# Kernel tuning notes

Measured on AMD Instinct MI355X. Metric: run time of the kernel, lower is better.

The kernel has to match this reference:

```python
import jax, jax.numpy as jnp
import numpy as np

N, E, F0, HEADS, B, OUT = 100000, 1600000, 128, 4, 64, 32
CHANNELS = [16, 8, 4, 2]
NEG_SLOPE = 0.2


def setup_inputs() -> dict:
    key = jax.random.key(0)
    ks = jax.random.split(key, 40)
    inp = {}
    inp['x'] = jax.random.normal(ks[0], (N, F0), dtype=jnp.float32)
    inp['edge_index'] = jax.random.randint(ks[1], (2, E), 0, N, dtype=jnp.int64)
    inp['batch'] = jnp.sort(jax.random.randint(ks[2], (N,), 0, B, dtype=jnp.int64))
    # GATConv params per layer: W [in, heads*out], att_src/att_dst [heads, out], bias [heads*out]
    in_dim = F0
    ki = 3
    for li, oc in enumerate(CHANNELS, start=1):
        scale = 1.0 / np.sqrt(in_dim)
        inp[f'W{li}'] = jax.random.normal(ks[ki], (in_dim, HEADS * oc), dtype=jnp.float32) * scale
        inp[f'a_src{li}'] = jax.random.normal(ks[ki + 1], (HEADS, oc), dtype=jnp.float32) * 0.1
        inp[f'a_dst{li}'] = jax.random.normal(ks[ki + 2], (HEADS, oc), dtype=jnp.float32) * 0.1
        inp[f'b{li}'] = jnp.zeros((HEADS * oc,), dtype=jnp.float32)
        ki += 3
        in_dim = HEADS * oc
    inp['W_fc'] = jax.random.normal(ks[ki], (2 * HEADS, OUT), dtype=jnp.float32) * (1.0 / np.sqrt(2 * HEADS))
    inp['b_fc'] = jnp.zeros((OUT,), dtype=jnp.float32)
    return inp


def gat_layer(x, src, dst, W, a_src, a_dst, b, oc):
    n = x.shape[0]
    h = (x @ W).reshape(n, HEADS, oc)                    # [N, H, C]
    al_s = jnp.einsum('nhc,hc->nh', h, a_src)            # [N, H]
    al_d = jnp.einsum('nhc,hc->nh', h, a_dst)
    e = jax.nn.leaky_relu(al_s[src] + al_d[dst], NEG_SLOPE)  # [E, H]
    # segment softmax over incoming edges per destination node
    m = jax.ops.segment_max(e, dst, num_segments=n)
    m = jnp.where(jnp.isfinite(m), m, 0.0)
    ex = jnp.exp(e - m[dst])
    s = jax.ops.segment_sum(ex, dst, num_segments=n)
    alpha = ex / (s[dst] + 1e-16)                        # [E, H]
    out = jax.ops.segment_sum(h[src] * alpha[:, :, None], dst, num_segments=n)
    return out.reshape(n, HEADS * oc) + b


def reference(x, edge_index, batch, W1, a_src1, a_dst1, b1, W2, a_src2, a_dst2, b2,
              W3, a_src3, a_dst3, b3, W4, a_src4, a_dst4, b4, W_fc, b_fc):
    n = x.shape[0]
    loops = jnp.arange(n, dtype=edge_index.dtype)
    src = jnp.concatenate([edge_index[0], loops])   # PyG GATConv adds self-loops
    dst = jnp.concatenate([edge_index[1], loops])
    params = [(W1, a_src1, a_dst1, b1), (W2, a_src2, a_dst2, b2),
              (W3, a_src3, a_dst3, b3), (W4, a_src4, a_dst4, b4)]
    h = x
    for (W, a_s, a_d, b), oc in zip(params, CHANNELS):
        h = jax.nn.relu(gat_layer(h, src, dst, W, a_s, a_d, b, oc))
        # dropout(0.3) is identity at inference
    # global mean pool over graphs in the batch
    sums = jax.ops.segment_sum(h, batch, num_segments=B)
    cnt = jax.ops.segment_sum(jnp.ones((n,), h.dtype), batch, num_segments=B)
    pooled = sums / jnp.maximum(cnt, 1.0)[:, None]
    return pooled @ W_fc + b_fc
```

## Files before the change

### kernel.cpp

```cpp
#include <hip/hip_runtime.h>
#include <hip/hip_bf16.h>

#define NNODES 100000
#define NEDGES 1600000
#define NHEADS 4
#define NGRAPH 64
#define NOUTF  32
#define BSH    9
#define NBUK   ((NNODES + 511) >> 9)
#define BPAD   16
#define BCAP   9216
#define CGRID  512
#define G1GRID ((NNODES + 63) / 64)

__device__ __forceinline__ unsigned short f2bf(float f) {
    union { float f; unsigned u; } v;
    v.f = f;
    unsigned r = v.u + 0x7FFF + ((v.u >> 16) & 1);
    return (unsigned short)(r >> 16);
}
__device__ __forceinline__ float bflo(unsigned u) {
    union { unsigned u; float f; } v;
    v.u = u << 16;
    return v.f;
// ... 40 lines not shown
            int d = wide ? ei[2 * (ne + i)] : ei[ne + i];
            atomicAdd(&hist[d >> BSH], 1);
        }
        __syncthreads();
        for (int i = tid; i < NBUK; i += 256)
            base[i] = hist[i] ? atomicAdd(&bkcur[i * BPAD], hist[i]) : 0;
        __syncthreads();
        for (int i = tid; i < NBUK; i += 256) hist[i] = 0;
        __syncthreads();
        for (int i = e0 + tid; i < e1; i += 256) {
            int s = wide ? ei[2 * i] : ei[i];
            int d = wide ? ei[2 * (ne + i)] : ei[ne + i];
            int bk = d >> BSH;
            int pos = base[bk] + atomicAdd(&hist[bk], 1);
            if (pos < BCAP) packed[bk * BCAP + pos] = s | ((d & 511) << 17);
        }
        int gid = blockIdx.x * 256 + tid;
        for (int i = gid; i < n; i += CGRID * 256) bat[i] = wide ? bt[2 * i] : bt[i];
    } else {
        constexpr int DIN = 128, DOUT = 64, KTILE = 64;
        constexpr int OG = DOUT / 4;
        constexpr int NPB = 64;
        constexpr int S = DIN + 4;
        constexpr int C = DOUT / NHEADS;
        float* Wl = smem;
        float* xs = smem + KTILE * DOUT;
        const int base = (blockIdx.x - CGRID) * NPB;
        constexpr int KC = DIN / 4;
        for (int i = tid; i < NPB * KC; i += 256) {
            int nn = i / KC, kc = i - nn * KC;
            int nd = base + nn;
            float4 v = (nd < n) ? ((const float4*)x)[(size_t)nd * KC + kc]
                                : make_float4(0.f, 0.f, 0.f, 0.f);
            *(float4*)&xs[nn * S + kc * 4] = v;
        }
        const int og = tid % OG;
        const int ng = tid / OG;
        const int n0 = ng * 4;
        float4 acc[4] = {};
        for (int kt = 0; kt < DIN; kt += KTILE) {
            __syncthreads();
            for (int i = tid; i < KTILE * OG; i += 256)
                ((float4*)Wl)[i] = ((const float4*)W1)[kt * OG + i];
            __syncthreads();
            #pragma unroll 2
            for (int k = 0; k < KTILE; k += 4) {
                float4 wv[4], xv[4];
                #pragma unroll
                for (int j = 0; j < 4; j++)
                    wv[j] = *(const float4*)&Wl[(k + j) * DOUT + og * 4];
                #pragma unroll
                for (int r = 0; r < 4; r++)
                    xv[r] = *(const float4*)&xs[(n0 + r) * S + kt + k];
                #pragma unroll
                for (int r = 0; r < 4; r++) {
                    fma4(acc[r], xv[r].x, wv[0]);
                    fma4(acc[r], xv[r].y, wv[1]);
                    fma4(acc[r], xv[r].z, wv[2]);
                    fma4(acc[r], xv[r].w, wv[3]);
                }
            }
        }
        float4 asv = ((const float4*)as1)[og];
        float4 adv = ((const float4*)ad1)[og];
        #pragma unroll
        for (int r = 0; r < 4; r++) {
            int node = base + n0 + r;
            bool ok = node < n;
            if (ok) {
                ushort4 o;
                o.x = f2bf(acc[r].x);
                o.y = f2bf(acc[r].y);
                o.z = f2bf(acc[r].z);
                o.w = f2bf(acc[r].w);
                ((ushort4*)h1)[(size_t)node * OG + og] = o;
            }
            float ps = acc[r].x * asv.x + acc[r].y * asv.y + acc[r].z * asv.z + acc[r].w * asv.w;
            float pd = acc[r].x * adv.x + acc[r].y * adv.y + acc[r].z * adv.z + acc[r].w * adv.w;
            #pragma unroll
            for (int off = 1; off < C / 4; off <<= 1) {
                ps += __shfl_xor(ps, off);
                pd += __shfl_xor(pd, off);
            }
            if (ok && (og % (C / 4)) == 0) {
                int hh = og / (C / 4);
                al_s[node * NHEADS + hh] = ps;
                al_d[node * NHEADS + hh] = pd;
            }
        }
    }
}

__global__ __launch_bounds__(1024) void gat_fine_kernel(
        const int* __restrict__ packed, const int* __restrict__ bkcur,
        int* __restrict__ row_ptr, int* __restrict__ col, int n) {
    __shared__ int bscan[256];
    __shared__ int dg[512];
    __shared__ int excl[512];
    __shared__ int partial[256];
    __shared__ int cur[512];
    int b = blockIdx.x;
    int tid = threadIdx.x;
    if (tid < 256) bscan[tid] = (tid < NBUK) ? bkcur[tid * BPAD] : 0;
    if (tid < 512) dg[tid] = 0;
    __syncthreads();
    for (int off = 1; off < 256; off <<= 1) {
        int u = (tid < 256 && tid >= off) ? bscan[tid - off] : 0;
        __syncthreads();
        if (tid < 256) bscan[tid] += u;
        __syncthreads();
    }
    int cntb = bkcur[b * BPAD];
    int csr0 = bscan[b] - cntb;
    int pbeg = b * BCAP;
    int pend = pbeg + cntb;
    for (int t = pbeg + tid; t < pend; t += 1024)
        atomicAdd(&dg[packed[t] >> 17], 1);
    __syncthreads();
    int a0 = 0, a1 = 0, s = 0;
    if (tid < 256) {
        a0 = dg[2 * tid];
        a1 = dg[2 * tid + 1];
        s = a0 + a1;
        partial[tid] = s;
    }
    __syncthreads();
    for (int off = 1; off < 256; off <<= 1) {
        int u = (tid < 256 && tid >= off) ? partial[tid - off] : 0;
        __syncthreads();
        if (tid < 256) partial[tid] += u;
        __syncthreads();
    }
    if (tid < 256) {
        int ebase = partial[tid] - s;
        excl[2 * tid] = ebase;
        excl[2 * tid + 1] = ebase + a0;
        cur[2 * tid] = ebase;
        cur[2 * tid + 1] = ebase + a0;
    }
    __syncthreads();
    int node0 = b << BSH;
    if (tid < 512) {
        int nd = node0 + tid;
        if (nd < n) row_ptr[nd] = csr0 + excl[tid];
    }
    if (b == NBUK - 1 && tid == 0) row_ptr[n] = bscan[NBUK - 1];
    for (int t = pbeg + tid; t < pend; t += 1024) {
        int v = packed[t];
        int pos = atomicAdd(&cur[v >> 17], 1);
        col[csr0 + pos] = v & 0x1FFFF;
    }
}

template<int DIN, int DOUT, int KTILE, bool BF16OUT, int STRIDE>
__global__ __launch_bounds__(256) void gat_gemm_attn_kernel(
        const float* __restrict__ in, const float* __restrict__ W,
        const float* __restrict__ a_src, const float* __restrict__ a_dst,
        char* __restrict__ hrow, float* __restrict__ al_d, int n) {
    constexpr int OG = DOUT / 4;
    constexpr int NPB = 1024 / OG;
    constexpr int S = DIN + 4;
    constexpr int C = DOUT / NHEADS;
    __shared__ float Wl[KTILE * DOUT];
    __shared__ float xs[NPB * S];
    const int tid = threadIdx.x;
    const int base = blockIdx.x * NPB;
    constexpr int KC = DIN / 4;
    for (int i = tid; i < NPB * KC; i += 256) {
        int nn = i / KC, kc = i - nn * KC;
        int nd = base + nn;
        float4 v = (nd < n) ? ((const float4*)in)[(size_t)nd * KC + kc]
                            : make_float4(0.f, 0.f, 0.f, 0.f);
        *(float4*)&xs[nn * S + kc * 4] = v;
    }
    const int og = tid % OG;
    const int ng = tid / OG;
    const int n0 = ng * 4;
    float4 acc[4] = {};
    for (int kt = 0; kt < DIN; kt += KTILE) {
        __syncthreads();
        for (int i = tid; i < KTILE * OG; i += 256)
            ((float4*)Wl)[i] = ((const float4*)W)[kt * OG + i];
        __syncthreads();
        #pragma unroll 2
        for (int k = 0; k < KTILE; k += 4) {
            float4 wv[4], xv[4];
            #pragma unroll
            for (int j = 0; j < 4; j++)
                wv[j] = *(const float4*)&Wl[(k + j) * DOUT + og * 4];
            #pragma unroll
            for (int r = 0; r < 4; r++)
                xv[r] = *(const float4*)&xs[(n0 + r) * S + kt + k];
            #pragma unroll
            for (int r = 0; r < 4; r++) {
                fma4(acc[r], xv[r].x, wv[0]);
                fma4(acc[r], xv[r].y, wv[1]);
                fma4(acc[r], xv[r].z, wv[2]);
                fma4(acc[r], xv[r].w, wv[3]);
            }
        }
    }
    float4 asv = ((const float4*)a_src)[og];
    float4 adv = ((const float4*)a_dst)[og];
    #pragma unroll
    for (int r = 0; r < 4; r++) {
        int node = base + n0 + r;
        bool ok = node < n;
        char* rp = hrow + (size_t)node * STRIDE;
        if (ok) {
            if constexpr (BF16OUT) {
                ushort4 o;
                o.x = f2bf(acc[r].x);
                o.y = f2bf(acc[r].y);
                o.z = f2bf(acc[r].z);
                o.w = f2bf(acc[r].w);
                *(ushort4*)(rp + 16 + og * 8) = o;
            } else {
                *(float4*)(rp + 16 + og * 16) = acc[r];
            }
        }
        if constexpr (C >= 4) {
            float ps = acc[r].x * asv.x + acc[r].y * asv.y + acc[r].z * asv.z + acc[r].w * asv.w;
            float pd = acc[r].x * adv.x + acc[r].y * adv.y + acc[r].z * adv.z + acc[r].w * adv.w;
            #pragma unroll
            for (int off = 1; off < C / 4; off <<= 1) {
                ps += __shfl_xor(ps, off);
                pd += __shfl_xor(pd, off);
            }
            if (ok && (og % (C / 4)) == 0) {
                int hh = og / (C / 4);
                *(float*)(rp + 4 * hh) = ps;
                al_d[node * NHEADS + hh] = pd;
            }
        } else {
            if (ok) {
                *(float*)(rp + 8 * og)     = acc[r].x * asv.x + acc[r].y * asv.y;
                *(float*)(rp + 8 * og + 4) = acc[r].z * asv.z + acc[r].w * asv.w;
                al_d[node * NHEADS + 2 * og]     = acc[r].x * adv.x + acc[r].y * adv.y;
                al_d[node * NHEADS + 2 * og + 1] = acc[r].z * adv.z + acc[r].w * adv.w;
            }
        }
    }
}

template<int G>
__global__ __launch_bounds__(256) void gat_agg_group_kernel(
        const unsigned short* __restrict__ h, const float* __restrict__ al_s,
        const float* __restrict__ al_d, const int* __restrict__ row_ptr,
        const int* __restrict__ col, const float* __restrict__ bias,
        float* __restrict__ out, int n) {
    constexpr int L = G / 8;
    constexpr int PW = 64 / L;
    constexpr int C = G / NHEADS;
    int lane = threadIdx.x & 63;
    int sub = lane & (L - 1);
    int gidx = lane / L;
    int node = blockIdx.x * (4 * PW) + (threadIdx.x >> 6) * PW + gidx;
    if (node >= n) return;
    int beg = row_ptr[node];
    int cnt = row_ptr[node + 1] - beg;
    const uint4* h4 = (const uint4*)h;
    float acc[8] = {};
    int j0 = sub * 8;
    const int hh = (sub * 8) / C;
    float ald = al_d[node * NHEADS + hh];
    float ws = 0.f;
    int total = cnt + 1;
    int t = 0;
    for (; t + 2 <= total; t += 2) {
        int s0 = col[beg + t];
        int s1 = (t + 1 < cnt) ? col[beg + t + 1] : node;
        float e0 = al_s[s0 * NHEADS + hh] + ald;
        float e1 = al_s[s1 * NHEADS + hh] + ald;
        uint4 hv0 = h4[(size_t)s0 * L + sub];
        uint4 hv1 = h4[(size_t)s1 * L + sub];
        e0 = (e0 > 0.f) ? e0 : 0.2f * e0;
        e1 = (e1 > 0.f) ? e1 : 0.2f * e1;
        float w0 = __expf(e0);
        float w1 = __expf(e1);
        ws += w0;
        acc[0] += w0 * bflo(hv0.x);
        acc[1] += w0 * bfhi(hv0.x);
        acc[2] += w0 * bflo(hv0.y);
        acc[3] += w0 * bfhi(hv0.y);
        acc[4] += w0 * bflo(hv0.z);
        acc[5] += w0 * bfhi(hv0.z);
        acc[6] += w0 * bflo(hv0.w);
        acc[7] += w0 * bfhi(hv0.w);
        ws += w1;
        acc[0] += w1 * bflo(hv1.x);
        acc[1] += w1 * bfhi(hv1.x);
        acc[2] += w1 * bflo(hv1.y);
        acc[3] += w1 * bfhi(hv1.y);
        acc[4] += w1 * bflo(hv1.z);
        acc[5] += w1 * bfhi(hv1.z);
        acc[6] += w1 * bflo(hv1.w);
        acc[7] += w1 * bfhi(hv1.w);
    }
    if (t < total) {
        int s0 = (t < cnt) ? col[beg + t] : node;
        float e0 = al_s[s0 * NHEADS + hh] + ald;
        uint4 hv0 = h4[(size_t)s0 * L + sub];
        e0 = (e0 > 0.f) ? e0 : 0.2f * e0;
        float w0 = __expf(e0);
        ws += w0;
        acc[0] += w0 * bflo(hv0.x);
        acc[1] += w0 * bfhi(hv0.x);
        acc[2] += w0 * bflo(hv0.y);
        acc[3] += w0 * bfhi(hv0.y);
        acc[4] += w0 * bflo(hv0.z);
        acc[5] += w0 * bfhi(hv0.z);
        acc[6] += w0 * bflo(hv0.w);
        acc[7] += w0 * bfhi(hv0.w);
    }
    float inv = 1.f / (ws + 1e-16f);
    #pragma unroll
    for (int k = 0; k < 8; k++) acc[k] = acc[k] * inv + bias[j0 + k];
    float4 o0, o1;
    o0.x = (acc[0] > 0.f) ? acc[0] : 0.f;
    o0.y = (acc[1] > 0.f) ? acc[1] : 0.f;
    o0.z = (acc[2] > 0.f) ? acc[2] : 0.f;
    o0.w = (acc[3] > 0.f) ? acc[3] : 0.f;
    o1.x = (acc[4] > 0.f) ? acc[4] : 0.f;
    o1.y = (acc[5] > 0.f) ? acc[5] : 0.f;
    o1.z = (acc[6] > 0.f) ? acc[6] : 0.f;
    o1.w = (acc[7] > 0.f) ? acc[7] : 0.f;
    *(float4*)&out[(size_t)node * G + j0] = o0;
    *(float4*)&out[(size_t)node * G + j0 + 4] = o1;
}

template<int G, int STRIDE>
__global__ __launch_bounds__(256) void gat_agg_row_kernel(
        const char* __restrict__ hrow, const float* __restrict__ al_d,
        const int* __restrict__ row_ptr, const int* __restrict__ col,
        const float* __restrict__ bias, float* __restrict__ out, int n) {
    constexpr int L = G / 8;
    constexpr int PW = 64 / L;
    constexpr int C = G / NHEADS;
    int lane = threadIdx.x & 63;
    int sub = lane & (L - 1);
    int gidx = lane / L;
    int node = blockIdx.x * (4 * PW) + (threadIdx.x >> 6) * PW + gidx;
    if (node >= n) return;
    int beg = row_ptr[node];
    int cnt = row_ptr[node + 1] - beg;
    float acc[8] = {};
    int j0 = sub * 8;
    if constexpr (C >= 8) {
        const int hh = sub;
        float ald = al_d[node * NHEADS + hh];
        float ws = 0.f;
        int total = cnt + 1;
        int t = 0;
        for (; t + 2 <= total; t += 2) {
            int s0 = col[beg + t];
            int s1 = (t + 1 < cnt) ? col[beg + t + 1] : node;
            const char* r0 = hrow + (size_t)s0 * STRIDE;
            const char* r1 = hrow + (size_t)s1 * STRIDE;
            float e0 = *(const float*)(r0 + 4 * hh) + ald;
            float e1 = *(const float*)(r1 + 4 * hh) + ald;
            uint4 hv0 = *(const uint4*)(r0 + 16 + 16 * sub);
            uint4 hv1 = *(const uint4*)(r1 + 16 + 16 * sub);
            e0 = (e0 > 0.f) ? e0 : 0.2f * e0;
            e1 = (e1 > 0.f) ? e1 : 0.2f * e1;
            float w0 = __expf(e0);
            float w1 = __expf(e1);
            ws += w0;
            acc[0] += w0 * bflo(hv0.x);
            acc[1] += w0 * bfhi(hv0.x);
            acc[2] += w0 * bflo(hv0.y);
            acc[3] += w0 * bfhi(hv0.y);
            acc[4] += w0 * bflo(hv0.z);
            acc[5] += w0 * bfhi(hv0.z);
            acc[6] += w0 * bflo(hv0.w);
            acc[7] += w0 * bfhi(hv0.w);
            ws += w1;
            acc[0] += w1 * bflo(hv1.x);
            acc[1] += w1 * bfhi(hv1.x);
            acc[2] += w1 * bflo(hv1.y);
            acc[3] += w1 * bfhi(hv1.y);
            acc[4] += w1 * bflo(hv1.z);
            acc[5] += w1 * bfhi(hv1.z);
            acc[6] += w1 * bflo(hv1.w);
            acc[7] += w1 * bfhi(hv1.w);
        }
        if (t < total) {
            int s0 = (t < cnt) ? col[beg + t] : node;
            const char* r0 = hrow + (size_t)s0 * STRIDE;
            float e0 = *(const float*)(r0 + 4 * hh) + ald;
            uint4 hv0 = *(const uint4*)(r0 + 16 + 16 * sub);
            e0 = (e0 > 0.f) ? e0 : 0.2f * e0;
            float w0 = __expf(e0);
            ws += w0;
            acc[0] += w0 * bflo(hv0.x);
            acc[1] += w0 * bfhi(hv0.x);
            acc[2] += w0 * bflo(hv0.y);
            acc[3] += w0 * bfhi(hv0.y);
            acc[4] += w0 * bflo(hv0.z);
            acc[5] += w0 * bfhi(hv0.z);
            acc[6] += w0 * bflo(hv0.w);
            acc[7] += w0 * bfhi(hv0.w);
        }
        float inv = 1.f / (ws + 1e-16f);
        #pragma unroll
        for (int k = 0; k < 8; k++) acc[k] = acc[k] * inv + bias[j0 + k];
    } else {
        const int hh0 = 2 * sub, hh1 = 2 * sub + 1;
        float ald0 = al_d[node * NHEADS + hh0];
        float ald1 = al_d[node * NHEADS + hh1];
        float ws0 = 0.f, ws1 = 0.f;
        int total = cnt + 1;
        int t = 0;
        for (; t + 2 <= total; t += 2) {
            int s0 = col[beg + t];
            int s1 = (t + 1 < cnt) ? col[beg + t + 1] : node;
            const char* r0 = hrow + (size_t)s0 * STRIDE;
            const char* r1 = hrow + (size_t)s1 * STRIDE;
            float2 a0 = *(const float2*)(r0 + 8 * sub);
            float2 a1 = *(const float2*)(r1 + 8 * sub);
            uint4 hv0 = *(const uint4*)(r0 + 16 + 16 * sub);
            uint4 hv1 = *(const uint4*)(r1 + 16 + 16 * sub);
            float e00 = a0.x + ald0;
            float e01 = a0.y + ald1;
            float e10 = a1.x + ald0;
            float e11 = a1.y + ald1;
            e00 = (e00 > 0.f) ? e00 : 0.2f * e00;
            e01 = (e01 > 0.f) ? e01 : 0.2f * e01;
            e10 = (e10 > 0.f) ? e10 : 0.2f * e10;
            e11 = (e11 > 0.f) ? e11 : 0.2f * e11;
            float w00 = __expf(e00);
            float w01 = __expf(e01);
            float w10 = __expf(e10);
            float w11 = __expf(e11);
            ws0 += w00;
            ws1 += w01;
            acc[0] += w00 * bflo(hv0.x);
            acc[1] += w00 * bfhi(hv0.x);
            acc[2] += w00 * bflo(hv0.y);
            acc[3] += w00 * bfhi(hv0.y);
            acc[4] += w01 * bflo(hv0.z);
            acc[5] += w01 * bfhi(hv0.z);
            acc[6] += w01 * bflo(hv0.w);
            acc[7] += w01 * bfhi(hv0.w);
            ws0 += w10;
            ws1 += w11;
            acc[0] += w10 * bflo(hv1.x);
            acc[1] += w10 * bfhi(hv1.x);
            acc[2] += w10 * bflo(hv1.y);
            acc[3] += w10 * bfhi(hv1.y);
            acc[4] += w11 * bflo(hv1.z);
            acc[5] += w11 * bfhi(hv1.z);
            acc[6] += w11 * bflo(hv1.w);
            acc[7] += w11 * bfhi(hv1.w);
        }
        if (t < total) {
            int s0 = (t < cnt) ? col[beg + t] : node;
            const char* r0 = hrow + (size_t)s0 * STRIDE;
            float2 a0 = *(const float2*)(r0 + 8 * sub);
            uint4 hv0 = *(const uint4*)(r0 + 16 + 16 * sub);
            float e00 = a0.x + ald0;
            float e01 = a0.y + ald1;
            e00 = (e00 > 0.f) ? e00 : 0.2f * e00;
            e01 = (e01 > 0.f) ? e01 : 0.2f * e01;
            float w00 = __expf(e00);
            float w01 = __expf(e01);
            ws0 += w00;
            ws1 += w01;
            acc[0] += w00 * bflo(hv0.x);
            acc[1] += w00 * bfhi(hv0.x);
            acc[2] += w00 * bflo(hv0.y);
            acc[3] += w00 * bfhi(hv0.y);
            acc[4] += w01 * bflo(hv0.z);
            acc[5] += w01 * bfhi(hv0.z);
            acc[6] += w01 * bflo(hv0.w);
            acc[7] += w01 * bfhi(hv0.w);
        }
        float inv0 = 1.f / (ws0 + 1e-16f);
        float inv1 = 1.f / (ws1 + 1e-16f);
        #pragma unroll
        for (int k = 0; k < 4; k++) acc[k] = acc[k] * inv0 + bias[j0 + k];
        #pragma unroll
        for (int k = 4; k < 8; k++) acc[k] = acc[k] * inv1 + bias[j0 + k];
    }
    float4 o0, o1;
    o0.x = (acc[0] > 0.f) ? acc[0] : 0.f;
    o0.y = (acc[1] > 0.f) ? acc[1] : 0.f;
    o0.z = (acc[2] > 0.f) ? acc[2] : 0.f;
    o0.w = (acc[3] > 0.f) ? acc[3] : 0.f;
    o1.x = (acc[4] > 0.f) ? acc[4] : 0.f;
    o1.y = (acc[5] > 0.f) ? acc[5] : 0.f;
    o1.z = (acc[6] > 0.f) ? acc[6] : 0.f;
    o1.w = (acc[7] > 0.f) ? acc[7] : 0.f;
    *(float4*)&out[(size_t)node * G + j0] = o0;
    *(float4*)&out[(size_t)node * G + j0 + 4] = o1;
}

__global__ __launch_bounds__(256) void gat_agg_f32row_kernel(
        const char* __restrict__ hrow, const float* __restrict__ al_d,
        const int* __restrict__ row_ptr, const int* __restrict__ col,
        const float* __restrict__ bias, float* __restrict__ out, int n) {
    constexpr int L = 2;
    constexpr int PW = 32;
    int lane = threadIdx.x & 63;
    int sub = lane & 1;
    int gidx = lane >> 1;
    int node = blockIdx.x * (4 * PW) + (threadIdx.x >> 6) * PW + gidx;
    if (node >= n) return;
    int beg = row_ptr[node];
    int cnt = row_ptr[node + 1] - beg;
    const int hh0 = 2 * sub, hh1 = 2 * sub + 1;
    float ald0 = al_d[node * NHEADS + hh0];
    float ald1 = al_d[node * NHEADS + hh1];
    float4 acc = make_float4(0.f, 0.f, 0.f, 0.f);
    float ws0 = 0.f, ws1 = 0.f;
    int total = cnt + 1;
    int t = 0;
    for (; t + 2 <= total; t += 2) {
        int s0 = col[beg + t];
        int s1 = (t + 1 < cnt) ? col[beg + t + 1] : node;
        const char* r0 = hrow + (size_t)s0 * 64;
        const char* r1 = hrow + (size_t)s1 * 64;
        float2 a0 = *(const float2*)(r0 + 8 * sub);
        float2 a1 = *(const float2*)(r1 + 8 * sub);
        float4 hv0 = *(const float4*)(r0 + 16 + 16 * sub);
        float4 hv1 = *(const float4*)(r1 + 16 + 16 * sub);
        float e00 = a0.x + ald0;
        float e01 = a0.y + ald1;
        float e10 = a1.x + ald0;
        float e11 = a1.y + ald1;
        e00 = (e00 > 0.f) ? e00 : 0.2f * e00;
        e01 = (e01 > 0.f) ? e01 : 0.2f * e01;
        e10 = (e10 > 0.f) ? e10 : 0.2f * e10;
        e11 = (e11 > 0.f) ? e11 : 0.2f * e11;
        float w00 = __expf(e00);
        float w01 = __expf(e01);
        float w10 = __expf(e10);
        float w11 = __expf(e11);
        ws0 += w00;
        ws1 += w01;
        acc.x += w00 * hv0.x;
        acc.y += w00 * hv0.y;
        acc.z += w01 * hv0.z;
        acc.w += w01 * hv0.w;
        ws0 += w10;
        ws1 += w11;
        acc.x += w10 * hv1.x;
        acc.y += w10 * hv1.y;
        acc.z += w11 * hv1.z;
        acc.w += w11 * hv1.w;
    }
    if (t < total) {
        int s0 = (t < cnt) ? col[beg + t] : node;
        const char* r0 = hrow + (size_t)s0 * 64;
        float2 a0 = *(const float2*)(r0 + 8 * sub);
        float4 hv0 = *(const float4*)(r0 + 16 + 16 * sub);
        float e00 = a0.x + ald0;
        float e01 = a0.y + ald1;
        e00 = (e00 > 0.f) ? e00 : 0.2f * e00;
        e01 = (e01 > 0.f) ? e01 : 0.2f * e01;
        float w00 = __expf(e00);
        float w01 = __expf(e01);
        ws0 += w00;
        ws1 += w01;
        acc.x += w00 * hv0.x;
        acc.y += w00 * hv0.y;
        acc.z += w01 * hv0.z;
        acc.w += w01 * hv0.w;
    }
    float4 bv = ((const float4*)bias)[sub];
    float4 v;
    v.x = acc.x / (ws0 + 1e-16f) + bv.x;
    v.y = acc.y / (ws0 + 1e-16f) + bv.y;
    v.z = acc.z / (ws1 + 1e-16f) + bv.z;
    v.w = acc.w / (ws1 + 1e-16f) + bv.w;
    v.x = (v.x > 0.f) ? v.x : 0.f;
    v.y = (v.y > 0.f) ? v.y : 0.f;
    v.z = (v.z > 0.f) ? v.z : 0.f;
    v.w = (v.w > 0.f) ? v.w : 0.f;
    ((float4*)out)[(size_t)node * L + sub] = v;
}

__global__ __launch_bounds__(256) void gat_poolfc_kernel(
        const float* __restrict__ x, const int* __restrict__ bat,
        const float* __restrict__ Wfc, const float* __restrict__ bfc,
        float* __restrict__ out, int n) {
    __shared__ float sh[256][9];
    int b = blockIdx.x;
    int tid = threadIdx.x;
    int lo = 0, hi = n;
    while (lo < hi) { int mid = (lo + hi) >> 1; if (bat[mid] < b) lo = mid + 1; else hi = mid; }
    int i0 = lo;
    hi = n;
    while (lo < hi) { int mid = (lo + hi) >> 1; if (bat[mid] < b + 1) lo = mid + 1; else hi = mid; }
    int i1 = lo;
    float a[8] = {};
    for (int i = i0 + tid; i < i1; i += 256) {
        float4 v0 = ((const float4*)x)[(size_t)i * 2];
        float4 v1 = ((const float4*)x)[(size_t)i * 2 + 1];
        a[0] += v0.x; a[1] += v0.y; a[2] += v0.z; a[3] += v0.w;
        a[4] += v1.x; a[5] += v1.y; a[6] += v1.z; a[7] += v1.w;
    }
    #pragma unroll
    for (int k = 0; k < 8; k++) sh[tid][k] = a[k];
    __syncthreads();
    for (int off = 128; off >= 1; off >>= 1) {
        if (tid < off)
            #pragma unroll
            for (int k = 0; k < 8; k++) sh[tid][k] += sh[tid + off][k];
        __syncthreads();
    }
    if (tid < NOUTF) {
        float c = (float)(i1 - i0);
        if (c < 1.f) c = 1.f;
        float acc = bfc[tid];
        #pragma unroll
        for (int d = 0; d < 8; d++) acc += (sh[0][d] / c) * Wfc[d * NOUTF + tid];
        out[b * NOUTF + tid] = acc;
    }
}

extern "C" void kernel_launch(void* const* d_in, const int* in_sizes, int n_in,
                              void* d_out, int out_size, void* d_ws, size_t ws_size,
                              hipStream_t stream) {
    const float* x = (const float*)d_in[0];
    const int* ei = (const int*)d_in[1];
    const int* batch = (const int*)d_in[2];
    const float* W1 = (const float*)d_in[3];
    const float* as1 = (const float*)d_in[4];
    const float* ad1 = (const float*)d_in[5];
    const float* b1 = (const float*)d_in[6];
    const float* W2 = (const float*)d_in[7];
    const float* as2 = (const float*)d_in[8];
    const float* ad2 = (const float*)d_in[9];
    const float* b2 = (const float*)d_in[10];
    const float* W3 = (const float*)d_in[11];
    const float* as3 = (const float*)d_in[12];
    const float* ad3 = (const float*)d_in[13];
    const float* b3 = (const float*)d_in[14];
    const float* W4 = (const float*)d_in[15];
    const float* as4 = (const float*)d_in[16];
    const float* ad4 = (const float*)d_in[17];
    const float* b4 = (const float*)d_in[18];
    const float* Wfc = (const float*)d_in[19];
    const float* bfc = (const float*)d_in[20];

    const int n = NNODES, ne = NEDGES;

    char* p = (char*)d_ws;
    auto carve = [&](size_t bytes) {
        char* r = p;
        p += (bytes + 255) & ~(size_t)255;
        return r;
    };
    int* row_ptr = (int*)carve((size_t)(n + 1) * 4);
    int* col = (int*)carve((size_t)ne * 4);
    int* bkcur = (int*)carve(256 * BPAD * 4);
    int* packed = (int*)carve((size_t)NBUK * BCAP * 4);
    float* buf_h = (float*)carve((size_t)n * 64 * 4);
    float* buf_x = (float*)carve((size_t)n * 64 * 4);
    float* al_s = (float*)carve((size_t)n * NHEADS * 4);
    float* al_d = (float*)carve((size_t)n * NHEADS * 4);
    int* bat = (int*)carve((size_t)n * 4);
    unsigned short* h_bf16 = (unsigned short*)buf_h;
    char* hrow = (char*)buf_h;

    hipMemsetAsync(bkcur, 0, 256 * BPAD * 4, stream);

    gat_coarse_gemm1_kernel<<<CGRID + G1GRID, 256, 0, stream>>>(
        ei, batch, bkcur, packed, bat, x, W1, as1, ad1, h_bf16, al_s, al_d, ne, n);

    gat_fine_kernel<<<NBUK, 1024, 0, stream>>>(packed, bkcur, row_ptr, col, n);

    gat_agg_group_kernel<64><<<(n + 31) / 32, 256, 0, stream>>>(
        h_bf16, al_s, al_d, row_ptr, col, b1, buf_x, n);

    gat_gemm_attn_kernel<64, 32, 64, true, 96><<<(n + 127) / 128, 256, 0, stream>>>(
        buf_x, W2, as2, ad2, hrow, al_d, n);
    gat_agg_row_kernel<32, 96><<<(n + 63) / 64, 256, 0, stream>>>(
        hrow, al_d, row_ptr, col, b2, buf_x, n);

    gat_gemm_attn_kernel<32, 16, 32, true, 64><<<(n + 255) / 256, 256, 0, stream>>>(
        buf_x, W3, as3, ad3, hrow, al_d, n);
    gat_agg_row_kernel<16, 64><<<(n + 127) / 128, 256, 0, stream>>>(
        hrow, al_d, row_ptr, col, b3, buf_x, n);

    gat_gemm_attn_kernel<16, 8, 16, false, 64><<<(n + 511) / 512, 256, 0, stream>>>(
        buf_x, W4, as4, ad4, hrow, al_d, n);
    gat_agg_f32row_kernel<<<(n + 127) / 128, 256, 0, stream>>>(
        hrow, al_d, row_ptr, col, b4, buf_x, n);

    gat_poolfc_kernel<<<NGRAPH, 256, 0, stream>>>(buf_x, bat, Wfc, bfc, (float*)d_out, n);
}
```

Measured before the change: 381.1 us.

## Fuse each layer's aggregation with the next layer's projection GEMM

Each layer's neighbour-aggregation kernel is merged with the following layer's dense projection and attention-logit computation. The aggregated, ReLU'd node row is written to shared memory and multiplied by the next weight matrix, which is also staged in shared memory. This removes the write and re-read of the intermediate activations in global memory and drops three kernel launches. In exchange the small GEMMs lose their cross-node register tiling. Output buffers now alternate between the two workspace buffers so a kernel never reads and writes the same one.

```diff
diff --git a/kernel.cpp b/kernel.cpp
--- a/kernel.cpp
+++ b/kernel.cpp
@@ -216,128 +216,44 @@
     }
 }
 
-template<int DIN, int DOUT, int KTILE, bool BF16OUT, int STRIDE>
-__global__ __launch_bounds__(256) void gat_gemm_attn_kernel(
-        const float* __restrict__ in, const float* __restrict__ W,
-        const float* __restrict__ a_src, const float* __restrict__ a_dst,
-        char* __restrict__ hrow, float* __restrict__ al_d, int n) {
-    constexpr int OG = DOUT / 4;
-    constexpr int NPB = 1024 / OG;
-    constexpr int S = DIN + 4;
-    constexpr int C = DOUT / NHEADS;
-    __shared__ float Wl[KTILE * DOUT];
-    __shared__ float xs[NPB * S];
+__global__ __launch_bounds__(256) void gat_agg1_gemm2_kernel(
+        const unsigned short* __restrict__ h, const float* __restrict__ al_s,
+        const float* __restrict__ al_d_l1, const int* __restrict__ row_ptr,
+        const int* __restrict__ col, const float* __restrict__ b1,
+        const float* __restrict__ W2, const float* __restrict__ as2,
+        const float* __restrict__ ad2, char* __restrict__ hrow_out,
+        float* __restrict__ al_d, int n) {
+    __shared__ float Wl[64 * 32];
+    __shared__ float xs[32 * 68];
     const int tid = threadIdx.x;
-    const int base = blockIdx.x * NPB;
-    constexpr int KC = DIN / 4;
-    for (int i = tid; i < NPB * KC; i += 256) {
-        int nn = i / KC, kc = i - nn * KC;
-        int nd = base + nn;
-        float4 v = (nd < n) ? ((const float4*)in)[(size_t)nd * KC + kc]
-                            : make_float4(0.f, 0.f, 0.f, 0.f);
-        *(float4*)&xs[nn * S + kc * 4] = v;
-    }
-    const int og = tid % OG;
-    const int ng = tid / OG;
-    const int n0 = ng * 4;
-    float4 acc[4] = {};
-    for (int kt = 0; kt < DIN; kt += KTILE) {
-        __syncthreads();
-        for (int i = tid; i < KTILE * OG; i += 256)
-            ((float4*)Wl)[i] = ((const float4*)W)[kt * OG + i];
-        __syncthreads();
-        #pragma unroll 2
-        for (int k = 0; k < KTILE; k += 4) {
-            float4 wv[4], xv[4];
-            #pragma unroll
-            for (int j = 0; j < 4; j++)
-                wv[j] = *(const float4*)&Wl[(k + j) * DOUT + og * 4];
-            #pragma unroll
-            for (int r = 0; r < 4; r++)
-                xv[r] = *(const float4*)&xs[(n0 + r) * S + kt + k];
-            #pragma unroll
-            for (int r = 0; r < 4; r++) {
-                fma4(acc[r], xv[r].x, wv[0]);
-                fma4(acc[r], xv[r].y, wv[1]);
-                fma4(acc[r], xv[r].z, wv[2]);
-                fma4(acc[r], xv[r].w, wv[3]);
-            }
-        }
-    }
-    float4 asv = ((const float4*)a_src)[og];
-    float4 adv = ((const float4*)a_dst)[og];
-    #pragma unroll
-    for (int r = 0; r < 4; r++) {
-        int node = base + n0 + r;
-        bool ok = node < n;
-        char* rp = hrow + (size_t)node * STRIDE;
-        if (ok) {
-            if constexpr (BF16OUT) {
-                ushort4 o;
-                o.x = f2bf(acc[r].x);
-                o.y = f2bf(acc[r].y);
-                o.z = f2bf(acc[r].z);
-                o.w = f2bf(acc[r].w);
-                *(ushort4*)(rp + 16 + og * 8) = o;
-            } else {
-                *(float4*)(rp + 16 + og * 16) = acc[r];
-            }
-        }
-        if constexpr (C >= 4) {
-            float ps = acc[r].x * asv.x + acc[r].y * asv.y + acc[r].z * asv.z + acc[r].w * asv.w;
-            float pd = acc[r].x * adv.x + acc[r].y * adv.y + acc[r].z * adv.z + acc[r].w * adv.w;
-            #pragma unroll
-            for (int off = 1; off < C / 4; off <<= 1) {
-                ps += __shfl_xor(ps, off);
-                pd += __shfl_xor(pd, off);
-            }
-            if (ok && (og % (C / 4)) == 0) {
-                int hh = og / (C / 4);
-                *(float*)(rp + 4 * hh) = ps;
-                al_d[node * NHEADS + hh] = pd;
-            }
-        } else {
-            if (ok) {
-                *(float*)(rp + 8 * og)     = acc[r].x * asv.x + acc[r].y * asv.y;
-                *(float*)(rp + 8 * og + 4) = acc[r].z * asv.z + acc[r].w * asv.w;
-                al_d[node * NHEADS + 2 * og]     = acc[r].x * adv.x + acc[r].y * adv.y;
-                al_d[node * NHEADS + 2 * og + 1] = acc[r].z * adv.z + acc[r].w * adv.w;
-            }
-        }
-    }
-}
-
-template<int G>
-__global__ __launch_bounds__(256) void gat_agg_group_kernel(
-        const unsigned short* __restrict__ h, const float* __restrict__ al_s,
-        const float* __restrict__ al_d, const int* __restrict__ row_ptr,
-        const int* __restrict__ col, const float* __restrict__ bias,
-        float* __restrict__ out, int n) {
-    constexpr int L = G / 8;
-    constexpr int PW = 64 / L;
-    constexpr int C = G / NHEADS;
-    int lane = threadIdx.x & 63;
-    int sub = lane & (L - 1);
-    int gidx = lane / L;
-    int node = blockIdx.x * (4 * PW) + (threadIdx.x >> 6) * PW + gidx;
-    if (node >= n) return;
-    int beg = row_ptr[node];
-    int cnt = row_ptr[node + 1] - beg;
+    for (int i = tid; i < 64 * 32 / 4; i += 256)
+        ((float4*)Wl)[i] = ((const float4*)W2)[i];
+    __syncthreads();
+    int lane = tid & 63;
+    int sub = lane & 7;
+    int gidx = lane >> 3;
+    int slot = (tid >> 6) * 8 + gidx;
+    int node = blockIdx.x * 32 + slot;
+    bool ok = node < n;
+    int node_c = ok ? node : (n - 1);
+    int beg = row_ptr[node_c];
+    int cnt = row_ptr[node_c + 1] - beg;
     const uint4* h4 = (const uint4*)h;
     float acc[8] = {};
     int j0 = sub * 8;
-    const int hh = (sub * 8) / C;
-    float ald = al_d[node * NHEADS + hh];
+    float ald = al_d_l1[node_c * NHEADS + sub];
+    ald = al_d_l1[node_c * NHEADS + (sub >> 1)];
+    const int hh = sub >> 1;
     float ws = 0.f;
     int total = cnt + 1;
     int t = 0;
     for (; t + 2 <= total; t += 2) {
         int s0 = col[beg + t];
-        int s1 = (t + 1 < cnt) ? col[beg + t + 1] : node;
+        int s1 = (t + 1 < cnt) ? col[beg + t + 1] : node_c;
         float e0 = al_s[s0 * NHEADS + hh] + ald;
         float e1 = al_s[s1 * NHEADS + hh] + ald;
-        uint4 hv0 = h4[(size_t)s0 * L + sub];
-        uint4 hv1 = h4[(size_t)s1 * L + sub];
+        uint4 hv0 = h4[(size_t)s0 * 8 + sub];
+        uint4 hv1 = h4[(size_t)s1 * 8 + sub];
         e0 = (e0 > 0.f) ? e0 : 0.2f * e0;
         e1 = (e1 > 0.f) ? e1 : 0.2f * e1;
         float w0 = __expf(e0);
@@ -362,9 +278,9 @@
         acc[7] += w1 * bfhi(hv1.w);
     }
     if (t < total) {
-        int s0 = (t < cnt) ? col[beg + t] : node;
+        int s0 = (t < cnt) ? col[beg + t] : node_c;
         float e0 = al_s[s0 * NHEADS + hh] + ald;
-        uint4 hv0 = h4[(size_t)s0 * L + sub];
+        uint4 hv0 = h4[(size_t)s0 * 8 + sub];
         e0 = (e0 > 0.f) ? e0 : 0.2f * e0;
         float w0 = __expf(e0);
         ws += w0;
@@ -379,184 +295,297 @@
     }
     float inv = 1.f / (ws + 1e-16f);
     #pragma unroll
-    for (int k = 0; k < 8; k++) acc[k] = acc[k] * inv + bias[j0 + k];
-    float4 o0, o1;
-    o0.x = (acc[0] > 0.f) ? acc[0] : 0.f;
-    o0.y = (acc[1] > 0.f) ? acc[1] : 0.f;
-    o0.z = (acc[2] > 0.f) ? acc[2] : 0.f;
-    o0.w = (acc[3] > 0.f) ? acc[3] : 0.f;
-    o1.x = (acc[4] > 0.f) ? acc[4] : 0.f;
-    o1.y = (acc[5] > 0.f) ? acc[5] : 0.f;
-    o1.z = (acc[6] > 0.f) ? acc[6] : 0.f;
-    o1.w = (acc[7] > 0.f) ? acc[7] : 0.f;
-    *(float4*)&out[(size_t)node * G + j0] = o0;
-    *(float4*)&out[(size_t)node * G + j0 + 4] = o1;
-}
-
-template<int G, int STRIDE>
-__global__ __launch_bounds__(256) void gat_agg_row_kernel(
-        const char* __restrict__ hrow, const float* __restrict__ al_d,
+    for (int k = 0; k < 8; k++) {
+        acc[k] = acc[k] * inv + b1[j0 + k];
+        acc[k] = (acc[k] > 0.f) ? acc[k] : 0.f;
+    }
+    float* xrow = &xs[slot * 68];
+    *(float4*)&xrow[j0] = make_float4(acc[0], acc[1], acc[2], acc[3]);
+    *(float4*)&xrow[j0 + 4] = make_float4(acc[4], acc[5], acc[6], acc[7]);
+    const float4* Wl4 = (const float4*)Wl;
+    float4 out4 = make_float4(0.f, 0.f, 0.f, 0.f);
+    #pragma unroll 4
+    for (int k = 0; k < 64; k += 4) {
+        float4 xv = *(const float4*)&xrow[k];
+        float4 w0 = Wl4[(k + 0) * 8 + sub];
+        float4 w1 = Wl4[(k + 1) * 8 + sub];
+        float4 w2 = Wl4[(k + 2) * 8 + sub];
+        float4 w3 = Wl4[(k + 3) * 8 + sub];
+        fma4(out4, xv.x, w0);
+        fma4(out4, xv.y, w1);
+        fma4(out4, xv.z, w2);
+        fma4(out4, xv.w, w3);
+    }
+    float4 asv = ((const float4*)as2)[sub];
+    float4 adv = ((const float4*)ad2)[sub];
+    char* rp = hrow_out + (size_t)node_c * 96;
+    if (ok) {
+        ushort4 o;
+        o.x = f2bf(out4.x);
+        o.y = f2bf(out4.y);
+        o.z = f2bf(out4.z);
+        o.w = f2bf(out4.w);
+        *(ushort4*)(rp + 16 + 8 * sub) = o;
+    }
+    float ps = out4.x * asv.x + out4.y * asv.y + out4.z * asv.z + out4.w * asv.w;
+    float pd = out4.x * adv.x + out4.y * adv.y + out4.z * adv.z + out4.w * adv.w;
+    ps += __shfl_xor(ps, 1);
+    pd += __shfl_xor(pd, 1);
+    if (ok && (sub & 1) == 0) {
+        int hh2 = sub >> 1;
+        *(float*)(rp + 4 * hh2) = ps;
+        al_d[node_c * NHEADS + hh2] = pd;
+    }
+}
+
+__global__ __launch_bounds__(256) void gat_agg2_gemm3_kernel(
+        const char* __restrict__ hrow, const float* __restrict__ al_d_in,
         const int* __restrict__ row_ptr, const int* __restrict__ col,
-        const float* __restrict__ bias, float* __restrict__ out, int n) {
-    constexpr int L = G / 8;
-    constexpr int PW = 64 / L;
-    constexpr int C = G / NHEADS;
-    int lane = threadIdx.x & 63;
-    int sub = lane & (L - 1);
-    int gidx = lane / L;
-    int node = blockIdx.x * (4 * PW) + (threadIdx.x >> 6) * PW + gidx;
-    if (node >= n) return;
-    int beg = row_ptr[node];
-    int cnt = row_ptr[node + 1] - beg;
+        const float* __restrict__ b2, const float* __restrict__ W3,
+        const float* __restrict__ as3, const float* __restrict__ ad3,
+        char* __restrict__ hrow_out, float* __restrict__ al_d, int n) {
+    __shared__ float Wl[32 * 16];
+    __shared__ float xs[64 * 36];
+    const int tid = threadIdx.x;
+    for (int i = tid; i < 32 * 16 / 4; i += 256)
+        ((float4*)Wl)[i] = ((const float4*)W3)[i];
+    __syncthreads();
+    int lane = tid & 63;
+    int sub = lane & 3;
+    int gidx = lane >> 2;
+    int slot = (tid >> 6) * 16 + gidx;
+    int node = blockIdx.x * 64 + slot;
+    bool ok = node < n;
+    int node_c = ok ? node : (n - 1);
+    int beg = row_ptr[node_c];
+    int cnt = row_ptr[node_c + 1] - beg;
     float acc[8] = {};
     int j0 = sub * 8;
-    if constexpr (C >= 8) {
-        const int hh = sub;
-        float ald = al_d[node * NHEADS + hh];
-        float ws = 0.f;
-        int total = cnt + 1;
-        int t = 0;
-        for (; t + 2 <= total; t += 2) {
-            int s0 = col[beg + t];
-            int s1 = (t + 1 < cnt) ? col[beg + t + 1] : node;
-            const char* r0 = hrow + (size_t)s0 * STRIDE;
-            const char* r1 = hrow + (size_t)s1 * STRIDE;
-            float e0 = *(const float*)(r0 + 4 * hh) + ald;
-            float e1 = *(const float*)(r1 + 4 * hh) + ald;
-            uint4 hv0 = *(const uint4*)(r0 + 16 + 16 * sub);
-            uint4 hv1 = *(const uint4*)(r1 + 16 + 16 * sub);
-            e0 = (e0 > 0.f) ? e0 : 0.2f * e0;
-            e1 = (e1 > 0.f) ? e1 : 0.2f * e1;
-            float w0 = __expf(e0);
-            float w1 = __expf(e1);
-            ws += w0;
-            acc[0] += w0 * bflo(hv0.x);
-            acc[1] += w0 * bfhi(hv0.x);
-            acc[2] += w0 * bflo(hv0.y);
-            acc[3] += w0 * bfhi(hv0.y);
-            acc[4] += w0 * bflo(hv0.z);
-            acc[5] += w0 * bfhi(hv0.z);
-            acc[6] += w0 * bflo(hv0.w);
-            acc[7] += w0 * bfhi(hv0.w);
-            ws += w1;
-            acc[0] += w1 * bflo(hv1.x);
-            acc[1] += w1 * bfhi(hv1.x);
-            acc[2] += w1 * bflo(hv1.y);
-            acc[3] += w1 * bfhi(hv1.y);
-            acc[4] += w1 * bflo(hv1.z);
-            acc[5] += w1 * bfhi(hv1.z);
-            acc[6] += w1 * bflo(hv1.w);
-            acc[7] += w1 * bfhi(hv1.w);
-        }
-        if (t < total) {
-            int s0 = (t < cnt) ? col[beg + t] : node;
-            const char* r0 = hrow + (size_t)s0 * STRIDE;
-            float e0 = *(const float*)(r0 + 4 * hh) + ald;
-            uint4 hv0 = *(const uint4*)(r0 + 16 + 16 * sub);
-            e0 = (e0 > 0.f) ? e0 : 0.2f * e0;
-            float w0 = __expf(e0);
-            ws += w0;
-            acc[0] += w0 * bflo(hv0.x);
-            acc[1] += w0 * bfhi(hv0.x);
-            acc[2] += w0 * bflo(hv0.y);
-            acc[3] += w0 * bfhi(hv0.y);
-            acc[4] += w0 * bflo(hv0.z);
-            acc[5] += w0 * bfhi(hv0.z);
-            acc[6] += w0 * bflo(hv0.w);
-            acc[7] += w0 * bfhi(hv0.w);
-        }
-        float inv = 1.f / (ws + 1e-16f);
-        #pragma unroll
-        for (int k = 0; k < 8; k++) acc[k] = acc[k] * inv + bias[j0 + k];
-    } else {
-        const int hh0 = 2 * sub, hh1 = 2 * sub + 1;
-        float ald0 = al_d[node * NHEADS + hh0];
-        float ald1 = al_d[node * NHEADS + hh1];
-        float ws0 = 0.f, ws1 = 0.f;
-        int total = cnt + 1;
-        int t = 0;
-        for (; t + 2 <= total; t += 2) {
-            int s0 = col[beg + t];
-            int s1 = (t + 1 < cnt) ? col[beg + t + 1] : node;
-            const char* r0 = hrow + (size_t)s0 * STRIDE;
-            const char* r1 = hrow + (size_t)s1 * STRIDE;
-            float2 a0 = *(const float2*)(r0 + 8 * sub);
-            float2 a1 = *(const float2*)(r1 + 8 * sub);
-            uint4 hv0 = *(const uint4*)(r0 + 16 + 16 * sub);
-            uint4 hv1 = *(const uint4*)(r1 + 16 + 16 * sub);
-            float e00 = a0.x + ald0;
-            float e01 = a0.y + ald1;
-            float e10 = a1.x + ald0;
-            float e11 = a1.y + ald1;
-            e00 = (e00 > 0.f) ? e00 : 0.2f * e00;
-            e01 = (e01 > 0.f) ? e01 : 0.2f * e01;
-            e10 = (e10 > 0.f) ? e10 : 0.2f * e10;
-            e11 = (e11 > 0.f) ? e11 : 0.2f * e11;
-            float w00 = __expf(e00);
-            float w01 = __expf(e01);
-            float w10 = __expf(e10);
-            float w11 = __expf(e11);
-            ws0 += w00;
-            ws1 += w01;
-            acc[0] += w00 * bflo(hv0.x);
-            acc[1] += w00 * bfhi(hv0.x);
-            acc[2] += w00 * bflo(hv0.y);
-            acc[3] += w00 * bfhi(hv0.y);
-            acc[4] += w01 * bflo(hv0.z);
-            acc[5] += w01 * bfhi(hv0.z);
-            acc[6] += w01 * bflo(hv0.w);
-            acc[7] += w01 * bfhi(hv0.w);
-            ws0 += w10;
-            ws1 += w11;
-            acc[0] += w10 * bflo(hv1.x);
-            acc[1] += w10 * bfhi(hv1.x);
-            acc[2] += w10 * bflo(hv1.y);
-            acc[3] += w10 * bfhi(hv1.y);
-            acc[4] += w11 * bflo(hv1.z);
-            acc[5] += w11 * bfhi(hv1.z);
-            acc[6] += w11 * bflo(hv1.w);
-            acc[7] += w11 * bfhi(hv1.w);
-        }
-        if (t < total) {
-            int s0 = (t < cnt) ? col[beg + t] : node;
-            const char* r0 = hrow + (size_t)s0 * STRIDE;
-            float2 a0 = *(const float2*)(r0 + 8 * sub);
-            uint4 hv0 = *(const uint4*)(r0 + 16 + 16 * sub);
-            float e00 = a0.x + ald0;
-            float e01 = a0.y + ald1;
-            e00 = (e00 > 0.f) ? e00 : 0.2f * e00;
-            e01 = (e01 > 0.f) ? e01 : 0.2f * e01;
-            float w00 = __expf(e00);
-            float w01 = __expf(e01);
-            ws0 += w00;
-            ws1 += w01;
-            acc[0] += w00 * bflo(hv0.x);
-            acc[1] += w00 * bfhi(hv0.x);
-            acc[2] += w00 * bflo(hv0.y);
-            acc[3] += w00 * bfhi(hv0.y);
-            acc[4] += w01 * bflo(hv0.z);
-            acc[5] += w01 * bfhi(hv0.z);
-            acc[6] += w01 * bflo(hv0.w);
-            acc[7] += w01 * bfhi(hv0.w);
-        }
-        float inv0 = 1.f / (ws0 + 1e-16f);
-        float inv1 = 1.f / (ws1 + 1e-16f);
-        #pragma unroll
-        for (int k = 0; k < 4; k++) acc[k] = acc[k] * inv0 + bias[j0 + k];
-        #pragma unroll
-        for (int k = 4; k < 8; k++) acc[k] = acc[k] * inv1 + bias[j0 + k];
-    }
-    float4 o0, o1;
-    o0.x = (acc[0] > 0.f) ? acc[0] : 0.f;
-    o0.y = (acc[1] > 0.f) ? acc[1] : 0.f;
-    o0.z = (acc[2] > 0.f) ? acc[2] : 0.f;
-    o0.w = (acc[3] > 0.f) ? acc[3] : 0.f;
-    o1.x = (acc[4] > 0.f) ? acc[4] : 0.f;
-    o1.y = (acc[5] > 0.f) ? acc[5] : 0.f;
-    o1.z = (acc[6] > 0.f) ? acc[6] : 0.f;
-    o1.w = (acc[7] > 0.f) ? acc[7] : 0.f;
-    *(float4*)&out[(size_t)node * G + j0] = o0;
-    *(float4*)&out[(size_t)node * G + j0 + 4] = o1;
+    const int hh = sub;
+    float ald = al_d_in[node_c * NHEADS + hh];
+    float ws = 0.f;
+    int total = cnt + 1;
+    int t = 0;
+    for (; t + 2 <= total; t += 2) {
+        int s0 = col[beg + t];
+        int s1 = (t + 1 < cnt) ? col[beg + t + 1] : node_c;
+        const char* r0 = hrow + (size_t)s0 * 96;
+        const char* r1 = hrow + (size_t)s1 * 96;
+        float e0 = *(const float*)(r0 + 4 * hh) + ald;
+        float e1 = *(const float*)(r1 + 4 * hh) + ald;
+        uint4 hv0 = *(const uint4*)(r0 + 16 + 16 * sub);
+        uint4 hv1 = *(const uint4*)(r1 + 16 + 16 * sub);
+        e0 = (e0 > 0.f) ? e0 : 0.2f * e0;
+        e1 = (e1 > 0.f) ? e1 : 0.2f * e1;
+        float w0 = __expf(e0);
+        float w1 = __expf(e1);
+        ws += w0;
+        acc[0] += w0 * bflo(hv0.x);
+        acc[1] += w0 * bfhi(hv0.x);
+        acc[2] += w0 * bflo(hv0.y);
+        acc[3] += w0 * bfhi(hv0.y);
+        acc[4] += w0 * bflo(hv0.z);
+        acc[5] += w0 * bfhi(hv0.z);
+        acc[6] += w0 * bflo(hv0.w);
+        acc[7] += w0 * bfhi(hv0.w);
+        ws += w1;
+        acc[0] += w1 * bflo(hv1.x);
+        acc[1] += w1 * bfhi(hv1.x);
+        acc[2] += w1 * bflo(hv1.y);
+        acc[3] += w1 * bfhi(hv1.y);
+        acc[4] += w1 * bflo(hv1.z);
+        acc[5] += w1 * bfhi(hv1.z);
+        acc[6] += w1 * bflo(hv1.w);
+        acc[7] += w1 * bfhi(hv1.w);
+    }
+    if (t < total) {
+        int s0 = (t < cnt) ? col[beg + t] : node_c;
+        const char* r0 = hrow + (size_t)s0 * 96;
+        float e0 = *(const float*)(r0 + 4 * hh) + ald;
+        uint4 hv0 = *(const uint4*)(r0 + 16 + 16 * sub);
+        e0 = (e0 > 0.f) ? e0 : 0.2f * e0;
+        float w0 = __expf(e0);
+        ws += w0;
+        acc[0] += w0 * bflo(hv0.x);
+        acc[1] += w0 * bfhi(hv0.x);
+        acc[2] += w0 * bflo(hv0.y);
+        acc[3] += w0 * bfhi(hv0.y);
+        acc[4] += w0 * bflo(hv0.z);
+        acc[5] += w0 * bfhi(hv0.z);
+        acc[6] += w0 * bflo(hv0.w);
+        acc[7] += w0 * bfhi(hv0.w);
+    }
+    float inv = 1.f / (ws + 1e-16f);
+    #pragma unroll
+    for (int k = 0; k < 8; k++) {
+        acc[k] = acc[k] * inv + b2[j0 + k];
+        acc[k] = (acc[k] > 0.f) ? acc[k] : 0.f;
+    }
+    float* xrow = &xs[slot * 36];
+    *(float4*)&xrow[j0] = make_float4(acc[0], acc[1], acc[2], acc[3]);
+    *(float4*)&xrow[j0 + 4] = make_float4(acc[4], acc[5], acc[6], acc[7]);
+    const float4* Wl4 = (const float4*)Wl;
+    float4 out4 = make_float4(0.f, 0.f, 0.f, 0.f);
+    #pragma unroll 4
+    for (int k = 0; k < 32; k += 4) {
+        float4 xv = *(const float4*)&xrow[k];
+        float4 w0 = Wl4[(k + 0) * 4 + sub];
+        float4 w1 = Wl4[(k + 1) * 4 + sub];
+        float4 w2 = Wl4[(k + 2) * 4 + sub];
+        float4 w3 = Wl4[(k + 3) * 4 + sub];
+        fma4(out4, xv.x, w0);
+        fma4(out4, xv.y, w1);
+        fma4(out4, xv.z, w2);
+        fma4(out4, xv.w, w3);
+    }
+    float4 asv = ((const float4*)as3)[sub];
+    float4 adv = ((const float4*)ad3)[sub];
+    char* rp = hrow_out + (size_t)node_c * 64;
+    if (ok) {
+        ushort4 o;
+        o.x = f2bf(out4.x);
+        o.y = f2bf(out4.y);
+        o.z = f2bf(out4.z);
+        o.w = f2bf(out4.w);
+        *(ushort4*)(rp + 16 + 8 * sub) = o;
+        float ps = out4.x * asv.x + out4.y * asv.y + out4.z * asv.z + out4.w * asv.w;
+        float pd = out4.x * adv.x + out4.y * adv.y + out4.z * adv.z + out4.w * adv.w;
+        *(float*)(rp + 4 * sub) = ps;
+        al_d[node_c * NHEADS + sub] = pd;
+    }
+}
+
+__global__ __launch_bounds__(256) void gat_agg3_gemm4_kernel(
+        const char* __restrict__ hrow, const float* __restrict__ al_d_in,
+        const int* __restrict__ row_ptr, const int* __restrict__ col,
+        const float* __restrict__ b3, const float* __restrict__ W4,
+        const float* __restrict__ as4, const float* __restrict__ ad4,
+        char* __restrict__ hrow_out, float* __restrict__ al_d, int n) {
+    __shared__ float Wl[16 * 8];
+    __shared__ float xs[128 * 20];
+    const int tid = threadIdx.x;
+    if (tid < 16 * 8 / 4) ((float4*)Wl)[tid] = ((const float4*)W4)[tid];
+    __syncthreads();
+    int lane = tid & 63;
+    int sub = lane & 1;
+    int gidx = lane >> 1;
+    int slot = (tid >> 6) * 32 + gidx;
+    int node = blockIdx.x * 128 + slot;
+    bool ok = node < n;
+    int node_c = ok ? node : (n - 1);
+    int beg = row_ptr[node_c];
+    int cnt = row_ptr[node_c + 1] - beg;
+    float acc[8] = {};
+    int j0 = sub * 8;
+    const int hh0 = 2 * sub, hh1 = 2 * sub + 1;
+    float ald0 = al_d_in[node_c * NHEADS + hh0];
+    float ald1 = al_d_in[node_c * NHEADS + hh1];
+    float ws0 = 0.f, ws1 = 0.f;
+    int total = cnt + 1;
+    int t = 0;
+    for (; t + 2 <= total; t += 2) {
+        int s0 = col[beg + t];
+        int s1 = (t + 1 < cnt) ? col[beg + t + 1] : node_c;
+        const char* r0 = hrow + (size_t)s0 * 64;
+        const char* r1 = hrow + (size_t)s1 * 64;
+        float2 a0 = *(const float2*)(r0 + 8 * sub);
+        float2 a1 = *(const float2*)(r1 + 8 * sub);
+        uint4 hv0 = *(const uint4*)(r0 + 16 + 16 * sub);
+        uint4 hv1 = *(const uint4*)(r1 + 16 + 16 * sub);
+        float e00 = a0.x + ald0;
+        float e01 = a0.y + ald1;
+        float e10 = a1.x + ald0;
+        float e11 = a1.y + ald1;
+        e00 = (e00 > 0.f) ? e00 : 0.2f * e00;
+        e01 = (e01 > 0.f) ? e01 : 0.2f * e01;
+        e10 = (e10 > 0.f) ? e10 : 0.2f * e10;
+        e11 = (e11 > 0.f) ? e11 : 0.2f * e11;
+        float w00 = __expf(e00);
+        float w01 = __expf(e01);
+        float w10 = __expf(e10);
+        float w11 = __expf(e11);
+        ws0 += w00;
+        ws1 += w01;
+        acc[0] += w00 * bflo(hv0.x);
+        acc[1] += w00 * bfhi(hv0.x);
+        acc[2] += w00 * bflo(hv0.y);
+        acc[3] += w00 * bfhi(hv0.y);
+        acc[4] += w01 * bflo(hv0.z);
+        acc[5] += w01 * bfhi(hv0.z);
+        acc[6] += w01 * bflo(hv0.w);
+        acc[7] += w01 * bfhi(hv0.w);
+        ws0 += w10;
+        ws1 += w11;
+        acc[0] += w10 * bflo(hv1.x);
+        acc[1] += w10 * bfhi(hv1.x);
+        acc[2] += w10 * bflo(hv1.y);
+        acc[3] += w10 * bfhi(hv1.y);
+        acc[4] += w11 * bflo(hv1.z);
+        acc[5] += w11 * bfhi(hv1.z);
+        acc[6] += w11 * bflo(hv1.w);
+        acc[7] += w11 * bfhi(hv1.w);
+    }
+    if (t < total) {
+        int s0 = (t < cnt) ? col[beg + t] : node_c;
+        const char* r0 = hrow + (size_t)s0 * 64;
+        float2 a0 = *(const float2*)(r0 + 8 * sub);
+        uint4 hv0 = *(const uint4*)(r0 + 16 + 16 * sub);
+        float e00 = a0.x + ald0;
+        float e01 = a0.y + ald1;
+        e00 = (e00 > 0.f) ? e00 : 0.2f * e00;
+        e01 = (e01 > 0.f) ? e01 : 0.2f * e01;
+        float w00 = __expf(e00);
+        float w01 = __expf(e01);
+        ws0 += w00;
+        ws1 += w01;
+        acc[0] += w00 * bflo(hv0.x);
+        acc[1] += w00 * bfhi(hv0.x);
+        acc[2] += w00 * bflo(hv0.y);
+        acc[3] += w00 * bfhi(hv0.y);
+        acc[4] += w01 * bflo(hv0.z);
+        acc[5] += w01 * bfhi(hv0.z);
+        acc[6] += w01 * bflo(hv0.w);
+        acc[7] += w01 * bfhi(hv0.w);
+    }
+    float inv0 = 1.f / (ws0 + 1e-16f);
+    float inv1 = 1.f / (ws1 + 1e-16f);
+    #pragma unroll
+    for (int k = 0; k < 4; k++) {
+        acc[k] = acc[k] * inv0 + b3[j0 + k];
+        acc[k] = (acc[k] > 0.f) ? acc[k] : 0.f;
+    }
+    #pragma unroll
+    for (int k = 4; k < 8; k++) {
+        acc[k] = acc[k] * inv1 + b3[j0 + k];
+        acc[k] = (acc[k] > 0.f) ? acc[k] : 0.f;
+    }
+    float* xrow = &xs[slot * 20];
+    *(float4*)&xrow[j0] = make_float4(acc[0], acc[1], acc[2], acc[3]);
+    *(float4*)&xrow[j0 + 4] = make_float4(acc[4], acc[5], acc[6], acc[7]);
+    const float4* Wl4 = (const float4*)Wl;
+    float4 out4 = make_float4(0.f, 0.f, 0.f, 0.f);
+    #pragma unroll
+    for (int k = 0; k < 16; k += 4) {
+        float4 xv = *(const float4*)&xrow[k];
+        float4 w0 = Wl4[(k + 0) * 2 + sub];
+        float4 w1 = Wl4[(k + 1) * 2 + sub];
+        float4 w2 = Wl4[(k + 2) * 2 + sub];
+        float4 w3 = Wl4[(k + 3) * 2 + sub];
+        fma4(out4, xv.x, w0);
+        fma4(out4, xv.y, w1);
+        fma4(out4, xv.z, w2);
+        fma4(out4, xv.w, w3);
+    }
+    float4 asv = ((const float4*)as4)[sub];
+    float4 adv = ((const float4*)ad4)[sub];
+    char* rp = hrow_out + (size_t)node_c * 64;
+    if (ok) {
+        *(float4*)(rp + 16 + 16 * sub) = out4;
+        *(float*)(rp + 8 * sub)     = out4.x * asv.x + out4.y * asv.y;
+        *(float*)(rp + 8 * sub + 4) = out4.z * asv.z + out4.w * asv.w;
+        al_d[node_c * NHEADS + 2 * sub]     = out4.x * adv.x + out4.y * adv.y;
+        al_d[node_c * NHEADS + 2 * sub + 1] = out4.z * adv.z + out4.w * adv.w;
+    }
 }
 
 __global__ __launch_bounds__(256) void gat_agg_f32row_kernel(
@@ -726,7 +755,6 @@
     float* al_d = (float*)carve((size_t)n * NHEADS * 4);
     int* bat = (int*)carve((size_t)n * 4);
     unsigned short* h_bf16 = (unsigned short*)buf_h;
-    char* hrow = (char*)buf_h;
 
     hipMemsetAsync(bkcur, 0, 256 * BPAD * 4, stream);
 
@@ -735,23 +763,17 @@
 
     gat_fine_kernel<<<NBUK, 1024, 0, stream>>>(packed, bkcur, row_ptr, col, n);
 
-    gat_agg_group_kernel<64><<<(n + 31) / 32, 256, 0, stream>>>(
-        h_bf16, al_s, al_d, row_ptr, col, b1, buf_x, n);
-
-    gat_gemm_attn_kernel<64, 32, 64, true, 96><<<(n + 127) / 128, 256, 0, stream>>>(
-        buf_x, W2, as2, ad2, hrow, al_d, n);
-    gat_agg_row_kernel<32, 96><<<(n + 63) / 64, 256, 0, stream>>>(
-        hrow, al_d, row_ptr, col, b2, buf_x, n);
-
-    gat_gemm_attn_kernel<32, 16, 32, true, 64><<<(n + 255) / 256, 256, 0, stream>>>(
-        buf_x, W3, as3, ad3, hrow, al_d, n);
-    gat_agg_row_kernel<16, 64><<<(n + 127) / 128, 256, 0, stream>>>(
-        hrow, al_d, row_ptr, col, b3, buf_x, n);
-
-    gat_gemm_attn_kernel<16, 8, 16, false, 64><<<(n + 511) / 512, 256, 0, stream>>>(
-        buf_x, W4, as4, ad4, hrow, al_d, n);
+    gat_agg1_gemm2_kernel<<<(n + 31) / 32, 256, 0, stream>>>(
+        h_bf16, al_s, al_d, row_ptr, col, b1, W2, as2, ad2, (char*)buf_x, al_d, n);
+
+    gat_agg2_gemm3_kernel<<<(n + 63) / 64, 256, 0, stream>>>(
+        (const char*)buf_x, al_d, row_ptr, col, b2, W3, as3, ad3, (char*)buf_h, al_d, n);
+
+    gat_agg3_gemm4_kernel<<<(n + 127) / 128, 256, 0, stream>>>(
+        (const char*)buf_h, al_d, row_ptr, col, b3, W4, as4, ad4, (char*)buf_x, al_d, n);
+
     gat_agg_f32row_kernel<<<(n + 127) / 128, 256, 0, stream>>>(
-        hrow, al_d, row_ptr, col, b4, buf_x, n);
-
-    gat_poolfc_kernel<<<NGRAPH, 256, 0, stream>>>(buf_x, bat, Wfc, bfc, (float*)d_out, n);
-}
+        (const char*)buf_x, al_d, row_ptr, col, b4, buf_h, n);
+
+    gat_poolfc_kernel<<<NGRAPH, 256, 0, stream>>>(buf_h, bat, Wfc, bfc, (float*)d_out, n);
+}
```

Result: faster. 345.0 us (-9.5%).
